# Optimization experiments

Measured on AMD Instinct MI355X. Metric: run time of the kernel, lower is better.

The kernel has to match this reference:

```python
import jax, jax.numpy as jnp
import numpy as np

B, D, H = 1024, 64, 128


def setup_inputs() -> dict:
    key = jax.random.key(0)
    ks = jax.random.split(key, 12)
    s1 = 1.0 / np.sqrt(4 * D)
    sh = 1.0 / np.sqrt(H)
    sd = 1.0 / np.sqrt(D)
    return {
        "x": jax.random.normal(ks[0], (B, D), dtype=jnp.float32),
        # edge_fn: Linear(4D,H) -> ReLU -> Linear(H,H)
        "W1": jax.random.uniform(ks[1], (4 * D, H), minval=-s1, maxval=s1, dtype=jnp.float32),
        "b1": jax.random.uniform(ks[2], (H,), minval=-s1, maxval=s1, dtype=jnp.float32),
        "W2": jax.random.uniform(ks[3], (H, H), minval=-sh, maxval=sh, dtype=jnp.float32),
        "b2": jax.random.uniform(ks[4], (H,), minval=-sh, maxval=sh, dtype=jnp.float32),
        # tau_proj: Linear(D,1) -> Softplus
        "Wt": jax.random.uniform(ks[5], (D, 1), minval=-sd, maxval=sd, dtype=jnp.float32),
        "bt": jax.random.uniform(ks[6], (1,), minval=-sd, maxval=sd, dtype=jnp.float32),
        # agg: Linear(H,H) -> ReLU
        "Wa": jax.random.uniform(ks[7], (H, H), minval=-sh, maxval=sh, dtype=jnp.float32),
        "ba": jax.random.uniform(ks[8], (H,), minval=-sh, maxval=sh, dtype=jnp.float32),
        # res_proj: Linear(D,H)
        "Wr": jax.random.uniform(ks[9], (D, H), minval=-sd, maxval=sd, dtype=jnp.float32),
        "br": jax.random.uniform(ks[10], (H,), minval=-sd, maxval=sd, dtype=jnp.float32),
        # LayerNorm(H)
        "gamma": jnp.ones((H,), dtype=jnp.float32),
        "beta": jnp.zeros((H,), dtype=jnp.float32),
    }


def reference(x, W1, b1, W2, b2, Wt, bt, Wa, ba, Wr, br, gamma, beta):
    d = x.shape[1]
    # Decompose first linear over concat([x_i, x_j, delta, |delta|]) into 4 sub-matmuls;
    # only the |delta| term needs the pairwise [B,B,D] tensor.
    Wi, Wj, Wd, Wab = W1[:d], W1[d:2 * d], W1[2 * d:3 * d], W1[3 * d:]
    ti = x @ Wi            # [B,H] (i-dependent)
    tj = x @ Wj            # [B,H] (j-dependent)
    td = x @ Wd            # [B,H] (delta = x_i - x_j contribution)
    delta = x[:, None, :] - x[None, :, :]             # [B,B,D]
    ta = jnp.einsum('ijd,dh->ijh', jnp.abs(delta), Wab)  # [B,B,H]
    pre = ti[:, None, :] + tj[None, :, :] + td[:, None, :] - td[None, :, :] + ta + b1
    d_proj = jax.nn.relu(pre) @ W2 + b2               # [B,B,H]
    tau = jnp.maximum(jax.nn.softplus(x @ Wt + bt), 0.01) + 1.0  # [B,1]
    h_mean = d_proj.mean(axis=1) / tau                # mean over j
    h = jax.nn.relu(h_mean @ Wa + ba)
    y = h + (x @ Wr + br)
    mu = y.mean(axis=-1, keepdims=True)
    var = ((y - mu) ** 2).mean(axis=-1, keepdims=True)  # biased, like torch LayerNorm
    return (y - mu) * jax.lax.rsqrt(var + 1e-5) * gamma + beta
```

## Files before the change

### kernel.cpp

```cpp
#include <hip/hip_runtime.h>
#include <hip/hip_bf16.h>
#include <math.h>

#define BB 1024
#define DD 64
#define HH 128

typedef _Float16 half8 __attribute__((ext_vector_type(8)));
typedef __fp16 fp16x2 __attribute__((ext_vector_type(2)));
typedef float floatx4 __attribute__((ext_vector_type(4)));

union H8 { fp16x2 p[4]; half8 v; };

__device__ __forceinline__ void async_cp16(const float* g, float* lds_wave_base) {
    __builtin_amdgcn_global_load_lds(
        (const __attribute__((address_space(1))) unsigned int*)g,
        (__attribute__((address_space(3))) unsigned int*)lds_wave_base,
        16, 0, 0);
}

__global__ __launch_bounds__(256) void prep_kernel(
    const float* __restrict__ x, const float* __restrict__ W1,
    const float* __restrict__ b1,
    float* __restrict__ c1, float* __restrict__ c2P,
    _Float16* __restrict__ wpack)
{
    __shared__ float xs[8][DD];
    const int t = threadIdx.x;
    const int i0 = blockIdx.x * 8;
    xs[t >> 6][t & 63] = x[i0 * DD + t];
    xs[4 + (t >> 6)][t & 63] = x[i0 * DD + 256 + t];
    __syncthreads();

    const int ii = t >> 5;
    const int h4 = t & 31;
    const int h = h4 * 4;
    const int i = i0 + ii;

    float4 a1 = {0.f, 0.f, 0.f, 0.f};
    float4 a2 = {0.f, 0.f, 0.f, 0.f};
    #pragma unroll 4
    for (int k = 0; k < DD; k++) {
        float4 wi = *(const float4*)(W1 + k * HH + h);
        float4 wj = *(const float4*)(W1 + (DD + k) * HH + h);
        float4 wd = *(const float4*)(W1 + (2 * DD + k) * HH + h);
        float xv = xs[ii][k];
        a1.x = fmaf(xv, wi.x + wd.x, a1.x);
        a1.y = fmaf(xv, wi.y + wd.y, a1.y);
        a1.z = fmaf(xv, wi.z + wd.z, a1.z);
        a1.w = fmaf(xv, wi.w + wd.w, a1.w);
        a2.x = fmaf(xv, wj.x - wd.x, a2.x);
        a2.y = fmaf(xv, wj.y - wd.y, a2.y);
        a2.z = fmaf(xv, wj.z - wd.z, a2.z);
        a2.w = fmaf(xv, wj.w - wd.w, a2.w);
    }
    float4 b1v = *(const float4*)(b1 + h);
    float4 c1v = {a1.x + b1v.x, a1.y + b1v.y, a1.z + b1v.z, a1.w + b1v.w};
    *(float4*)(c1 + i * HH + h) = c1v;

    const int jl = i & 15;
    float* cb = c2P + (i >> 4) * 2048 + (h >> 6) * 1024 + ((h >> 4) & 3) * 256 + (jl & 3);
    const int p0 = (jl >> 2) * 16 + (h & 15);
    cb[(p0 + 0) * 4] = a2.x;
    cb[(p0 + 1) * 4] = a2.y;
    cb[(p0 + 2) * 4] = a2.z;
    cb[(p0 + 3) * 4] = a2.w;

    if (blockIdx.x < 32) {
        int f = blockIdx.x * 256 + t;
        int jj = f & 7;
        int l  = (f >> 3) & 63;
        int u  = f >> 9;
        int s  = u & 1, t4 = (u >> 1) & 3, hh = u >> 3;
        int k  = s * 32 + ((l >> 4) << 3) + jj;
        int hcol = hh * 64 + t4 * 16 + (l & 15);
        wpack[f] = (_Float16)W1[(3 * DD + k) * HH + hcol];
    }
}

__global__ __launch_bounds__(256, 4) void pair_kernel(
    const float* __restrict__ x, const float* __restrict__ c1,
    const float* __restrict__ c2P, const _Float16* __restrict__ wpack,
    float* __restrict__ Sp)
{
    __shared__ __align__(16) float xs[2][1024];
    __shared__ __align__(16) float c2s[2][1024];

    const int t = threadIdx.x;
    const int wave = t >> 6;
    const int l = t & 63;
    const int quad = l >> 4, lm = l & 15;
    const int bid = blockIdx.x;
    const int ig = bid >> 3;
    const int hh = (bid >> 2) & 1;
    const int jq = bid & 3;
    const int i = ig * 4 + wave;
    const int j0base = jq * 256;
    const int sw = lm & 7;

    async_cp16(x + (j0base + (t >> 4)) * DD + (((t & 15) ^ ((t >> 4) & 7)) << 2),
               &xs[0][0] + wave * 256);
    async_cp16(c2P + (j0base >> 4) * 2048 + hh * 1024 + t * 4,
               &c2s[0][0] + wave * 256);

    float xi[16];
    {
        const float* xg = x + i * DD + quad * 8;
        *(float4*)(xi)      = *(const float4*)(xg);
        *(float4*)(xi + 4)  = *(const float4*)(xg + 4);
        *(float4*)(xi + 8)  = *(const float4*)(xg + 32);
        *(float4*)(xi + 12) = *(const float4*)(xg + 36);
    }
    float c1r[4];
    #pragma unroll
    for (int t4 = 0; t4 < 4; t4++)
        c1r[t4] = c1[i * HH + hh * 64 + t4 * 16 + lm];
    half8 wf[8];
    #pragma unroll
    for (int u = 0; u < 8; u++)
        wf[u] = *(const half8*)(wpack + ((hh * 8 + u) * 64 + l) * 8);

    float S[4] = {0.f, 0.f, 0.f, 0.f};

    for (int tile = 0; tile < 16; ++tile) {
        const int cur = tile & 1;
        __syncthreads();

        if (tile < 15) {
            const int jn = j0base + (tile + 1) * 16;
            async_cp16(x + (jn + (t >> 4)) * DD + (((t & 15) ^ ((t >> 4) & 7)) << 2),
                       &xs[cur ^ 1][0] + wave * 256);
            async_cp16(c2P + (jn >> 4) * 2048 + hh * 1024 + t * 4,
                       &c2s[cur ^ 1][0] + wave * 256);
        }

        floatx4 acc[4];
        #pragma unroll
        for (int t4 = 0; t4 < 4; t4++) {
            float4 c2v = *(const float4*)(&c2s[cur][t4 * 256 + l * 4]);
            acc[t4][0] = c2v.x + c1r[t4];
            acc[t4][1] = c2v.y + c1r[t4];
            acc[t4][2] = c2v.z + c1r[t4];
            acc[t4][3] = c2v.w + c1r[t4];
        }

        const float* xb = &xs[cur][lm * 64];
        float4 a0 = *(const float4*)(xb + (((quad * 2)     ^ sw) << 2));
        float4 a1 = *(const float4*)(xb + (((quad * 2 + 1) ^ sw) << 2));
        float4 a2 = *(const float4*)(xb + (((quad * 2 + 8) ^ sw) << 2));
        float4 a3 = *(const float4*)(xb + (((quad * 2 + 9) ^ sw) << 2));
        H8 af0, af1;
        af0.p[0] = __builtin_amdgcn_cvt_pkrtz(fabsf(xi[0] - a0.x),  fabsf(xi[1] - a0.y));
        af0.p[1] = __builtin_amdgcn_cvt_pkrtz(fabsf(xi[2] - a0.z),  fabsf(xi[3] - a0.w));
        af0.p[2] = __builtin_amdgcn_cvt_pkrtz(fabsf(xi[4] - a1.x),  fabsf(xi[5] - a1.y));
        af0.p[3] = __builtin_amdgcn_cvt_pkrtz(fabsf(xi[6] - a1.z),  fabsf(xi[7] - a1.w));
        af1.p[0] = __builtin_amdgcn_cvt_pkrtz(fabsf(xi[8] - a2.x),  fabsf(xi[9] - a2.y));
        af1.p[1] = __builtin_amdgcn_cvt_pkrtz(fabsf(xi[10] - a2.z), fabsf(xi[11] - a2.w));
        af1.p[2] = __builtin_amdgcn_cvt_pkrtz(fabsf(xi[12] - a3.x), fabsf(xi[13] - a3.y));
        af1.p[3] = __builtin_amdgcn_cvt_pkrtz(fabsf(xi[14] - a3.z), fabsf(xi[15] - a3.w));

        #pragma unroll
        for (int t4 = 0; t4 < 4; t4++) {
            acc[t4] = __builtin_amdgcn_mfma_f32_16x16x32_f16(af0.v, wf[t4 * 2 + 0], acc[t4], 0, 0, 0);
            acc[t4] = __builtin_amdgcn_mfma_f32_16x16x32_f16(af1.v, wf[t4 * 2 + 1], acc[t4], 0, 0, 0);
        }
        #pragma unroll
        for (int t4 = 0; t4 < 4; t4++) {
            S[t4] += fmaxf(acc[t4][0], 0.f);
            S[t4] += fmaxf(acc[t4][1], 0.f);
            S[t4] += fmaxf(acc[t4][2], 0.f);
            S[t4] += fmaxf(acc[t4][3], 0.f);
        }
    }

    #pragma unroll
    for (int t4 = 0; t4 < 4; t4++) {
        S[t4] += __shfl_xor(S[t4], 16, 64);
        S[t4] += __shfl_xor(S[t4], 32, 64);
    }
    if (quad == 0) {
        #pragma unroll
        for (int t4 = 0; t4 < 4; t4++)
            Sp[(jq * BB + i) * HH + hh * 64 + t4 * 16 + lm] = S[t4];
    }
}

__global__ __launch_bounds__(256) void finish_kernel(
    const float* __restrict__ Sp, const float* __restrict__ W2,
    const float* __restrict__ b2, const float* __restrict__ x,
    const float* __restrict__ Wt, const float* __restrict__ bt,
    const float* __restrict__ Wa, const float* __restrict__ ba,
    const float* __restrict__ Wr, const float* __restrict__ br,
    const float* __restrict__ gamma, const float* __restrict__ beta,
    float* __restrict__ out)
{
    __shared__ float Srow[8][HH];
    __shared__ float mrow[8][HH];
    __shared__ float xrowS[8][DD];
    __shared__ float taus[8];
    const int t = threadIdx.x;
    const int ii = t >> 5;
    const int h4 = t & 31;
    const int h = h4 * 4;
    const int i0 = blockIdx.x * 8;
    const int i = i0 + ii;

    {
        float4 s = {0.f, 0.f, 0.f, 0.f};
        #pragma unroll
        for (int q = 0; q < 4; q++) {
            float4 v = *(const float4*)(Sp + (q * BB + i) * HH + h);
            s.x += v.x; s.y += v.y; s.z += v.z; s.w += v.w;
        }
        const float inv = 1.0f / (float)BB;
        float4 sm = {s.x * inv, s.y * inv, s.z * inv, s.w * inv};
        *(float4*)(&Srow[ii][h]) = sm;
    }
    xrowS[t >> 6][t & 63] = x[i0 * DD + t];
    xrowS[4 + (t >> 6)][t & 63] = x[i0 * DD + 256 + t];

    {
        float p = x[i * DD + h4] * Wt[h4] + x[i * DD + 32 + h4] * Wt[32 + h4];
        #pragma unroll
        for (int off = 16; off; off >>= 1) p += __shfl_xor(p, off, 64);
        if (h4 == 0) {
            float z = p + bt[0];
            float sp = (z > 20.f) ? z : log1pf(expf(z));
            taus[ii] = fmaxf(sp, 0.01f) + 1.0f;
        }
    }
    __syncthreads();

    float4 acc = *(const float4*)(b2 + h);
    #pragma unroll 8
    for (int k = 0; k < HH; k++) {
        float4 w = *(const float4*)(W2 + k * HH + h);
        float sv = Srow[ii][k];
        acc.x = fmaf(sv, w.x, acc.x); acc.y = fmaf(sv, w.y, acc.y);
        acc.z = fmaf(sv, w.z, acc.z); acc.w = fmaf(sv, w.w, acc.w);
    }
    const float itau = 1.0f / taus[ii];
    float4 mv = {acc.x * itau, acc.y * itau, acc.z * itau, acc.w * itau};
    *(float4*)(&mrow[ii][h]) = mv;
    __syncthreads();

    float4 a2 = *(const float4*)(ba + h);
    #pragma unroll 8
    for (int k = 0; k < HH; k++) {
        float4 w = *(const float4*)(Wa + k * HH + h);
        float sv = mrow[ii][k];
        a2.x = fmaf(sv, w.x, a2.x); a2.y = fmaf(sv, w.y, a2.y);
        a2.z = fmaf(sv, w.z, a2.z); a2.w = fmaf(sv, w.w, a2.w);
    }
    float4 brv = *(const float4*)(br + h);
    float4 y = {fmaxf(a2.x, 0.f) + brv.x, fmaxf(a2.y, 0.f) + brv.y,
                fmaxf(a2.z, 0.f) + brv.z, fmaxf(a2.w, 0.f) + brv.w};
    #pragma unroll 8
    for (int d = 0; d < DD; d++) {
        float4 w = *(const float4*)(Wr + d * HH + h);
        float xv = xrowS[ii][d];
        y.x = fmaf(xv, w.x, y.x); y.y = fmaf(xv, w.y, y.y);
        y.z = fmaf(xv, w.z, y.z); y.w = fmaf(xv, w.w, y.w);
    }

    float p = y.x + y.y + y.z + y.w;
    #pragma unroll
    for (int off = 16; off; off >>= 1) p += __shfl_xor(p, off, 64);
    float mu = p * (1.0f / (float)HH);
    float4 dy = {y.x - mu, y.y - mu, y.z - mu, y.w - mu};
    float q = dy.x * dy.x + dy.y * dy.y + dy.z * dy.z + dy.w * dy.w;
    #pragma unroll
    for (int off = 16; off; off >>= 1) q += __shfl_xor(q, off, 64);
    float rs = rsqrtf(q * (1.0f / (float)HH) + 1e-5f);
    float4 gv = *(const float4*)(gamma + h);
    float4 bv = *(const float4*)(beta + h);
    float4 o = {dy.x * rs * gv.x + bv.x, dy.y * rs * gv.y + bv.y,
                dy.z * rs * gv.z + bv.z, dy.w * rs * gv.w + bv.w};
    *(float4*)(out + i * HH + h) = o;
}

extern "C" void kernel_launch(void* const* d_in, const int* in_sizes, int n_in,
                              void* d_out, int out_size, void* d_ws, size_t ws_size,
                              hipStream_t stream)
{
    const float* x     = (const float*)d_in[0];
    const float* W1    = (const float*)d_in[1];
    const float* b1    = (const float*)d_in[2];
    const float* W2    = (const float*)d_in[3];
    const float* b2    = (const float*)d_in[4];
    const float* Wt    = (const float*)d_in[5];
    const float* bt    = (const float*)d_in[6];
    const float* Wa    = (const float*)d_in[7];
    const float* ba    = (const float*)d_in[8];
    const float* Wr    = (const float*)d_in[9];
    const float* br    = (const float*)d_in[10];
    const float* gamma = (const float*)d_in[11];
    const float* beta  = (const float*)d_in[12];
    float* out = (float*)d_out;

    char* ws = (char*)d_ws;
    float*     c1    = (float*)(ws);
    float*     c2P   = (float*)(ws + (512 << 10));
    _Float16*  wpack = (_Float16*)(ws + (1024 << 10));
    float*     Sp    = (float*)(ws + (1056 << 10));

    prep_kernel<<<128, 256, 0, stream>>>(x, W1, b1, c1, c2P, wpack);
    pair_kernel<<<2048, 256, 0, stream>>>(x, c1, c2P, wpack, Sp);
    finish_kernel<<<128, 256, 0, stream>>>(Sp, W2, b2, x, Wt, bt,
                                           Wa, ba, Wr, br, gamma, beta, out);
}
```

Measured before the change: 133.7 us.

## Stage x as fp16 and compute packed fp16 abs-diff in pair kernel

The prep kernel now also writes an fp16 copy of x, and the pair kernel loads that copy into LDS, halving the staged x bytes per tile. The |x_i - x_j| fragments are computed with packed fp16 subtraction and a sign-bit mask, replacing the fp32 subtract, fabs and convert sequence. Async copies are split by wave, with two waves loading x and two loading c2. The cost is precision: the difference is now taken in fp16 rather than in fp32 and then rounded, which may add error for close values.

```diff
diff --git a/kernel.cpp b/kernel.cpp
--- a/kernel.cpp
+++ b/kernel.cpp
@@ -7,12 +7,18 @@
 #define HH 128
 
 typedef _Float16 half8 __attribute__((ext_vector_type(8)));
-typedef __fp16 fp16x2 __attribute__((ext_vector_type(2)));
+typedef _Float16 f16x2 __attribute__((ext_vector_type(2)));
 typedef float floatx4 __attribute__((ext_vector_type(4)));
 
-union H8 { fp16x2 p[4]; half8 v; };
-
-__device__ __forceinline__ void async_cp16(const float* g, float* lds_wave_base) {
+union PKU { unsigned u[4]; f16x2 h[4]; half8 v; uint4 q; };
+
+__device__ __forceinline__ unsigned pk_absdiff(f16x2 a, f16x2 b) {
+    union { f16x2 h; unsigned u; } c;
+    c.h = a - b;
+    return c.u & 0x7FFF7FFFu;
+}
+
+__device__ __forceinline__ void async_cp16(const void* g, void* lds_wave_base) {
     __builtin_amdgcn_global_load_lds(
         (const __attribute__((address_space(1))) unsigned int*)g,
         (__attribute__((address_space(3))) unsigned int*)lds_wave_base,
@@ -23,13 +29,19 @@
     const float* __restrict__ x, const float* __restrict__ W1,
     const float* __restrict__ b1,
     float* __restrict__ c1, float* __restrict__ c2P,
-    _Float16* __restrict__ wpack)
+    _Float16* __restrict__ wpack, _Float16* __restrict__ xh)
 {
     __shared__ float xs[8][DD];
     const int t = threadIdx.x;
     const int i0 = blockIdx.x * 8;
-    xs[t >> 6][t & 63] = x[i0 * DD + t];
-    xs[4 + (t >> 6)][t & 63] = x[i0 * DD + 256 + t];
+    {
+        float v0 = x[i0 * DD + t];
+        float v1 = x[i0 * DD + 256 + t];
+        xs[t >> 6][t & 63] = v0;
+        xs[4 + (t >> 6)][t & 63] = v1;
+        xh[i0 * DD + t] = (_Float16)v0;
+        xh[i0 * DD + 256 + t] = (_Float16)v1;
+    }
     __syncthreads();
 
     const int ii = t >> 5;
@@ -79,11 +91,11 @@
 }
 
 __global__ __launch_bounds__(256, 4) void pair_kernel(
-    const float* __restrict__ x, const float* __restrict__ c1,
-    const float* __restrict__ c2P, const _Float16* __restrict__ wpack,
+    const float* __restrict__ c1, const float* __restrict__ c2P,
+    const _Float16* __restrict__ wpack, const _Float16* __restrict__ xh,
     float* __restrict__ Sp)
 {
-    __shared__ __align__(16) float xs[2][1024];
+    __shared__ __align__(16) _Float16 xsh[2][1024];
     __shared__ __align__(16) float c2s[2][1024];
 
     const int t = threadIdx.x;
@@ -98,19 +110,30 @@
     const int j0base = jq * 256;
     const int sw = lm & 7;
 
-    async_cp16(x + (j0base + (t >> 4)) * DD + (((t & 15) ^ ((t >> 4) & 7)) << 2),
-               &xs[0][0] + wave * 256);
-    async_cp16(c2P + (j0base >> 4) * 2048 + hh * 1024 + t * 4,
-               &c2s[0][0] + wave * 256);
-
-    float xi[16];
-    {
-        const float* xg = x + i * DD + quad * 8;
-        *(float4*)(xi)      = *(const float4*)(xg);
-        *(float4*)(xi + 4)  = *(const float4*)(xg + 4);
-        *(float4*)(xi + 8)  = *(const float4*)(xg + 32);
-        *(float4*)(xi + 12) = *(const float4*)(xg + 36);
-    }
+    const _Float16* xsrc = nullptr;
+    const float* csrc = nullptr;
+    if (wave < 2) {
+        int g = t;
+        int j = g >> 3, p = g & 7;
+        int c = p ^ (j & 7);
+        xsrc = xh + (j0base + j) * DD + c * 8;
+    } else {
+        int s = (wave - 2) * 2;
+        csrc = c2P + (j0base >> 4) * 2048 + hh * 1024 + s * 256 + l * 4;
+    }
+
+    if (wave < 2) {
+        async_cp16(xsrc, (char*)&xsh[0][0] + wave * 1024);
+    } else {
+        int s = (wave - 2) * 2;
+        async_cp16(csrc,       &c2s[0][0] + s * 256);
+        async_cp16(csrc + 256, &c2s[0][0] + (s + 1) * 256);
+    }
+
+    PKU xi0, xi1;
+    xi0.q = *(const uint4*)(xh + i * DD + quad * 8);
+    xi1.q = *(const uint4*)(xh + i * DD + 32 + quad * 8);
+
     float c1r[4];
     #pragma unroll
     for (int t4 = 0; t4 < 4; t4++)
@@ -122,16 +145,24 @@
 
     float S[4] = {0.f, 0.f, 0.f, 0.f};
 
+    const int rp0 = quad ^ sw;
+    const int rp1 = (quad + 4) ^ sw;
+
+    #pragma unroll 1
     for (int tile = 0; tile < 16; ++tile) {
         const int cur = tile & 1;
         __syncthreads();
 
         if (tile < 15) {
-            const int jn = j0base + (tile + 1) * 16;
-            async_cp16(x + (jn + (t >> 4)) * DD + (((t & 15) ^ ((t >> 4) & 7)) << 2),
-                       &xs[cur ^ 1][0] + wave * 256);
-            async_cp16(c2P + (jn >> 4) * 2048 + hh * 1024 + t * 4,
-                       &c2s[cur ^ 1][0] + wave * 256);
+            if (wave < 2) {
+                xsrc += 16 * DD;
+                async_cp16(xsrc, (char*)&xsh[cur ^ 1][0] + wave * 1024);
+            } else {
+                csrc += 2048;
+                int s = (wave - 2) * 2;
+                async_cp16(csrc,       &c2s[cur ^ 1][0] + s * 256);
+                async_cp16(csrc + 256, &c2s[cur ^ 1][0] + (s + 1) * 256);
+            }
         }
 
         floatx4 acc[4];
@@ -144,20 +175,16 @@
             acc[t4][3] = c2v.w + c1r[t4];
         }
 
-        const float* xb = &xs[cur][lm * 64];
-        float4 a0 = *(const float4*)(xb + (((quad * 2)     ^ sw) << 2));
-        float4 a1 = *(const float4*)(xb + (((quad * 2 + 1) ^ sw) << 2));
-        float4 a2 = *(const float4*)(xb + (((quad * 2 + 8) ^ sw) << 2));
-        float4 a3 = *(const float4*)(xb + (((quad * 2 + 9) ^ sw) << 2));
-        H8 af0, af1;
-        af0.p[0] = __builtin_amdgcn_cvt_pkrtz(fabsf(xi[0] - a0.x),  fabsf(xi[1] - a0.y));
-        af0.p[1] = __builtin_amdgcn_cvt_pkrtz(fabsf(xi[2] - a0.z),  fabsf(xi[3] - a0.w));
-        af0.p[2] = __builtin_amdgcn_cvt_pkrtz(fabsf(xi[4] - a1.x),  fabsf(xi[5] - a1.y));
-        af0.p[3] = __builtin_amdgcn_cvt_pkrtz(fabsf(xi[6] - a1.z),  fabsf(xi[7] - a1.w));
-        af1.p[0] = __builtin_amdgcn_cvt_pkrtz(fabsf(xi[8] - a2.x),  fabsf(xi[9] - a2.y));
-        af1.p[1] = __builtin_amdgcn_cvt_pkrtz(fabsf(xi[10] - a2.z), fabsf(xi[11] - a2.w));
-        af1.p[2] = __builtin_amdgcn_cvt_pkrtz(fabsf(xi[12] - a3.x), fabsf(xi[13] - a3.y));
-        af1.p[3] = __builtin_amdgcn_cvt_pkrtz(fabsf(xi[14] - a3.z), fabsf(xi[15] - a3.w));
+        const _Float16* xb = &xsh[cur][lm * 64];
+        PKU t0, t1;
+        t0.q = *(const uint4*)(xb + rp0 * 8);
+        t1.q = *(const uint4*)(xb + rp1 * 8);
+        PKU af0, af1;
+        #pragma unroll
+        for (int r = 0; r < 4; r++) {
+            af0.u[r] = pk_absdiff(t0.h[r], xi0.h[r]);
+            af1.u[r] = pk_absdiff(t1.h[r], xi1.h[r]);
+        }
 
         #pragma unroll
         for (int t4 = 0; t4 < 4; t4++) {
@@ -302,10 +329,11 @@
     float*     c1    = (float*)(ws);
     float*     c2P   = (float*)(ws + (512 << 10));
     _Float16*  wpack = (_Float16*)(ws + (1024 << 10));
-    float*     Sp    = (float*)(ws + (1056 << 10));
-
-    prep_kernel<<<128, 256, 0, stream>>>(x, W1, b1, c1, c2P, wpack);
-    pair_kernel<<<2048, 256, 0, stream>>>(x, c1, c2P, wpack, Sp);
+    _Float16*  xh    = (_Float16*)(ws + (1040 << 10));
+    float*     Sp    = (float*)(ws + (1168 << 10));
+
+    prep_kernel<<<128, 256, 0, stream>>>(x, W1, b1, c1, c2P, wpack, xh);
+    pair_kernel<<<2048, 256, 0, stream>>>(c1, c2P, wpack, xh, Sp);
     finish_kernel<<<128, 256, 0, stream>>>(Sp, W2, b2, x, Wt, bt,
                                            Wa, ba, Wr, br, gamma, beta, out);
 }
```

New measurement: 135.3 us. No clear change (+1.2%).
